# Kernel tuning notes

Measured on AMD Instinct MI355X. Metric: run time of the kernel, lower is better.

Reference implementation:

```python
import jax, jax.numpy as jnp
import numpy as np

W, E, D, NL, NC = 2048, 256, 512, 4, 5
DI, DS, DR, DC = 1024, 64, 32, 4  # d_inner=2*D, d_state, dt_rank=ceil(D/16), d_conv


def setup_inputs() -> dict:
    key = jax.random.key(0)
    ks = jax.random.split(key, 24)
    s = 0.02
    byte_sequence = jax.random.randint(ks[0], (2, W), 0, 256, dtype=jnp.int32)
    p = {
        "byte_sequence": byte_sequence,
        "byte_embed": jax.random.normal(ks[1], (256, E)) * s,
        "pos_embed": jax.random.normal(ks[2], (W, E)) * s,
        "in_w": jax.random.normal(ks[3], (D, E)) * s,
        "in_b": jnp.zeros((D,)),
        "ln_g": jnp.ones((NL, D)),
        "ln_b": jnp.zeros((NL, D)),
        "m_in_w": jax.random.normal(ks[4], (NL, 2 * DI, D)) * s,
        "conv_w": jax.random.normal(ks[5], (NL, DI, DC)) * s,
        "conv_b": jnp.zeros((NL, DI)),
        "xp_w": jax.random.normal(ks[6], (NL, DR + 2 * DS, DI)) * s,
        "dt_w": jax.random.normal(ks[7], (NL, DI, DR)) * s,
        "dt_b": jnp.full((NL, DI), -4.6),  # softplus(-4.6) ~ 0.01, in [dt_min, dt_max]
        "A_log": jnp.broadcast_to(jnp.log(jnp.arange(1.0, DS + 1.0)), (NL, DI, DS)) + 0.0,
        "Dp": jnp.ones((NL, DI)),
        "m_out_w": jax.random.normal(ks[8], (NL, D, DI)) * s,
        "h1_w": jax.random.normal(ks[9], (256, D)) * s,
        "h1_b": jnp.zeros((256,)),
        "h2_w": jax.random.normal(ks[10], (128, 256)) * s,
        "h2_b": jnp.zeros((128,)),
        "h3_w": jax.random.normal(ks[11], (NC, 128)) * s,
        "h3_b": jnp.zeros((NC,)),
    }
    return p


def _layernorm(x, g, b, eps=1e-5):
    mu = jnp.mean(x, axis=-1, keepdims=True)
    var = jnp.mean((x - mu) ** 2, axis=-1, keepdims=True)
    return (x - mu) * jax.lax.rsqrt(var + eps) * g + b


def _mamba(x, in_w, cw, cb, xp_w, dt_w, dt_b, A_log, Dp_, out_w):
    B, L, _ = x.shape
    xr = x @ in_w.T                       # [B,L,2*DI]
    xs, res = xr[..., :DI], xr[..., DI:]
    # causal depthwise conv1d over L
    xc = jnp.transpose(xs, (0, 2, 1))     # [B,DI,L]
    xc = jax.lax.conv_general_dilated(xc, cw[:, None, :], (1,), [(DC - 1, 0)], feature_group_count=DI)
    xs = jax.nn.silu(jnp.transpose(xc + cb[None, :, None], (0, 2, 1)))  # [B,L,DI]
    xdbl = xs @ xp_w.T                    # [B,L,DR+2*DS]
    dt, Bm, Cm = xdbl[..., :DR], xdbl[..., DR:DR + DS], xdbl[..., DR + DS:]
    delta = jax.nn.softplus(dt @ dt_w.T + dt_b)  # [B,L,DI]
    A = -jnp.exp(A_log)                   # [DI,DS]

    def step(h, inp):
        d_t, B_t, C_t, x_t = inp          # [B,DI],[B,DS],[B,DS],[B,DI]
        dA = jnp.exp(d_t[:, :, None] * A)             # [B,DI,DS]
        h = dA * h + (d_t * x_t)[:, :, None] * B_t[:, None, :]
        y = jnp.einsum('bds,bs->bd', h, C_t)
        return h, y

    h0 = jnp.zeros((B, DI, DS), x.dtype)
    seq = (jnp.swapaxes(delta, 0, 1), jnp.swapaxes(Bm, 0, 1), jnp.swapaxes(Cm, 0, 1), jnp.swapaxes(xs, 0, 1))
    _, ys = jax.lax.scan(step, h0, seq)   # ys: [L,B,DI]
    y = jnp.swapaxes(ys, 0, 1) + xs * Dp_
    y = y * jax.nn.silu(res)
    return y @ out_w.T


def reference(byte_sequence, byte_embed, pos_embed, in_w, in_b, ln_g, ln_b, m_in_w, conv_w, conv_b, xp_w, dt_w, dt_b, A_log, Dp, m_out_w, h1_w, h1_b, h2_w, h2_b, h3_w, h3_b):
    B, L = byte_sequence.shape
    x = byte_embed[byte_sequence] + pos_embed[None, :L]  # [B,L,E]
    x = x @ in_w.T + in_b                                # [B,L,D]
    for i in range(NL):
        res = x
        h = _layernorm(x, ln_g[i], ln_b[i])
        h = _mamba(h, m_in_w[i], conv_w[i], conv_b[i], xp_w[i], dt_w[i], dt_b[i], A_log[i], Dp[i], m_out_w[i])
        x = h + res
    h = jax.nn.relu(x @ h1_w.T + h1_b)
    h = jax.nn.relu(h @ h2_w.T + h2_b)
    return h @ h3_w.T + h3_b
```

## Files before the change

### kernel.cpp

```cpp
#include <hip/hip_runtime.h>
#include <hip/hip_bf16.h>

#define WLEN 2048
#define EDIM 256
#define DDIM 512
#define NLAYER 4
#define NCLS 5
#define DI 1024
#define DS 64
#define DR 32
#define DC 4
#define BB 2
#define TOK (BB*WLEN)
#define XD (DR + 2*DS)
#define CL 128
#define NCH (WLEN/CL)
#define LOG2E 1.44269504f

typedef __bf16 bf16x8 __attribute__((ext_vector_type(8)));
typedef float  f32x4  __attribute__((ext_vector_type(4)));

static __device__ __forceinline__ unsigned short f2bf(float f) {
    union { float f; unsigned u; } v; v.f = f;
    unsigned r = v.u + 0x7fffu + ((v.u >> 16) & 1u);
    return (unsigned short)(r >> 16);
}

__global__ __launch_bounds__(256) void embed_k(const int* __restrict__ seq,
    const float* __restrict__ be, const float* __restrict__ pe,
    float* __restrict__ out)
{
    int idx = blockIdx.x * 256 + threadIdx.x;
    int e  = idx & (EDIM - 1);
    int bl = idx >> 8;
    int l  = bl & (WLEN - 1);
    int tok = seq[bl];
    out[idx] = be[tok * EDIM + e] + pe[l * EDIM + e];
}

__global__ __launch_bounds__(256) void ln_k(const float* __restrict__ x,
    const float* __restrict__ g, const float* __restrict__ b,
    unsigned short* __restrict__ out)
{
    int row  = blockIdx.x * 4 + (threadIdx.x >> 6);
    int lane = threadIdx.x & 63;
    const float* xp = x + (size_t)row * DDIM;
    float v[8];
    float s = 0.f;
#pragma unroll
    for (int i = 0; i < 8; i++) { v[i] = xp[lane + 64 * i]; s += v[i]; }
#pragma unroll
    for (int off = 32; off; off >>= 1) s += __shfl_xor(s, off, 64);
    float mu = s * (1.f / 512.f);
    float s2 = 0.f;
#pragma unroll
    for (int i = 0; i < 8; i++) { float d = v[i] - mu; s2 += d * d; }
#pragma unroll
    for (int off = 32; off; off >>= 1) s2 += __shfl_xor(s2, off, 64);
    float rs = rsqrtf(s2 * (1.f / 512.f) + 1e-5f);
#pragma unroll
    for (int i = 0; i < 8; i++) {
        int c = lane + 64 * i;
        out[(size_t)row * DDIM + c] = f2bf((v[i] - mu) * rs * g[c] + b[c]);
    }
}

__global__ __launch_bounds__(256) void conv_silu_k(const float* __restrict__ xr,
    const float* __restrict__ cw, const float* __restrict__ cb,
    float* __restrict__ xs)
{
    int idx = blockIdx.x * 256 + threadIdx.x;
    int d  = idx & (DI - 1);
    int bl = idx >> 10;
    int l  = bl & (WLEN - 1);
    float acc = cb[d];
    const float* wp = cw + d * DC;
#pragma unroll
    for (int k = 0; k < DC; k++) {
        int ls = l - (DC - 1) + k;
        if (ls >= 0)
            acc = fmaf(xr[((size_t)(bl - (DC - 1) + k)) * (2 * DI) + d], wp[k], acc);
    }
    xs[idx] = acc / (1.f + __expf(-acc));
}

__global__ __launch_bounds__(256) void f2bf_k(const float* __restrict__ in,
    unsigned short* __restrict__ out, int n)
{
    int i = blockIdx.x * 256 + threadIdx.x;
    if (i < n) out[i] = f2bf(in[i]);
}

__global__ __launch_bounds__(256) void trans_CT_k(const float* __restrict__ xdbl,
    float* __restrict__ CT)
{
    __shared__ float tile[64][65];
    int bt = blockIdx.x, b = blockIdx.z;
    int col = threadIdx.x & 63, rr = threadIdx.x >> 6;
#pragma unroll
    for (int k = 0; k < 16; k++) {
        int i = k * 4 + rr;
        tile[i][col] = xdbl[((size_t)(b * WLEN + bt * 64 + i)) * XD + DR + DS + col];
    }
    __syncthreads();
#pragma unroll
    for (int k = 0; k < 16; k++) {
        int ss = k * 4 + rr;
        CT[((size_t)(b * DS + ss)) * WLEN + bt * 64 + col] = tile[col][ss];
    }
}

__global__ __launch_bounds__(256) void trans_y_k(const float* __restrict__ yT,
    unsigned short* __restrict__ ybf)
{
    __shared__ float tile[64][65];
    int bt = blockIdx.x, bd = blockIdx.y, b = blockIdx.z;
    int col = threadIdx.x & 63, rr = threadIdx.x >> 6;
#pragma unroll
    for (int k = 0; k < 16; k++) {
        int i = k * 4 + rr;
        tile[i][col] = yT[((size_t)(b * DI + bd * 64 + i)) * WLEN + bt * 64 + col];
    }
    __syncthreads();
#pragma unroll
    for (int k = 0; k < 16; k++) {
        int tt = k * 4 + rr;
        ybf[((size_t)(b * WLEN + bt * 64 + tt)) * DI + bd * 64 + col] = f2bf(tile[col][tt]);
    }
}

#define SU 8

#define LOADG1(T0, dlt, xv, Bt, Ct)                                      \
  _Pragma("unroll")                                                      \
  for (int u = 0; u < SU; u++) {                                         \
    size_t bl = base + (size_t)(T0) + u;                                 \
    dlt[u] = delta[bl * DI + d];                                         \
    xv[u]  = xs[bl * DI + d];                                            \
    Bt[u]  = xdbl[bl * XD + DR + lane];                                  \
    Ct[u]  = xdbl[bl * XD + DR + DS + lane];                             \
  }

#define COMPG1(T0, dlt, xv, Bt, Ct)                                      \
  {                                                                      \
    float dA[SU], p[SU], cds[SU];                                        \
    _Pragma("unroll")                                                    \
    for (int u = 0; u < SU; u++) dA[u] = __expf(dlt[u] * Aa);            \
    _Pragma("unroll")                                                    \
    for (int u = 0; u < SU; u++) {                                       \
      hst = fmaf(dA[u], hst, dlt[u] * xv[u] * Bt[u]);                    \
      p[u] = hst * Ct[u];                                                \
    }                                                                    \
    if (lane == 0) {                                                     \
      _Pragma("unroll")                                                  \
      for (int u = 0; u < SU; u++) p[u] = fmaf(xv[u], Dpd, p[u]);        \
    }                                                                    \
    cds[0] = cd + dlt[0];                                                \
    _Pragma("unroll")                                                    \
    for (int u = 1; u < SU; u++) cds[u] = cds[u - 1] + dlt[u];           \
    cd = cds[SU - 1];                                                    \
    _Pragma("unroll")                                                    \
    for (int u = 0; u < SU; u++)                                         \
      if (lane == u) cdT[tbase + (size_t)(T0) + u] = cds[u];             \
    _Pragma("unroll")                                                    \
    for (int u = 0; u < SU; u++) wred[u * 64 + lane] = p[u];             \
    float4 q0 = *(const float4*)&wred[(lane >> 3) * 64 + (lane & 7) * 8];     \
    float4 q1 = *(const float4*)&wred[(lane >> 3) * 64 + (lane & 7) * 8 + 4]; \
    float sred = ((q0.x + q0.y) + (q0.z + q0.w)) +                       \
                 ((q1.x + q1.y) + (q1.z + q1.w));                        \
    sred += __shfl_xor(sred, 1, 64);                                     \
    sred += __shfl_xor(sred, 2, 64);                                     \
    sred += __shfl_xor(sred, 4, 64);                                     \
    if ((lane & 7) == 0) zT[tbase + (size_t)(T0) + (lane >> 3)] = sred;  \
  }

__global__ __launch_bounds__(256) void scan1_k(
    const float* __restrict__ delta,
    const float* __restrict__ xdbl,
    const float* __restrict__ xs,
    const float* __restrict__ A_log,
    const float* __restrict__ Dp,
    float* __restrict__ zT,
    float* __restrict__ cdT,
    float* __restrict__ Hbuf,
    float* __restrict__ Sbuf)
{
    __shared__ float red[4 * SU * 64];
    int wv   = threadIdx.x >> 6;
    float* wred = red + wv * (SU * 64);
    int wid  = blockIdx.x * 4 + wv;
    int lane = threadIdx.x & 63;
    int c  = wid & (NCH - 1);
    int bd = wid >> 4;
    int d  = bd & (DI - 1);
    float Aa  = -__expf(A_log[d * DS + lane]);
    float Dpd = Dp[d];
    float hst = 0.f, cd = 0.f;
    size_t base  = (size_t)(bd >> 10) * WLEN + (size_t)c * CL;
    size_t tbase = (size_t)bd * WLEN + (size_t)c * CL;

    float da[SU], xa[SU], Ba[SU], Ca[SU];
    float db[SU], xb[SU], Bb[SU], Cb[SU];

    LOADG1(0, da, xa, Ba, Ca)
    for (int t0 = 0; t0 < CL; t0 += 2 * SU) {
        LOADG1(t0 + SU, db, xb, Bb, Cb)
        COMPG1(t0, da, xa, Ba, Ca)
        if (t0 + 2 * SU < CL)
            LOADG1(t0 + 2 * SU, da, xa, Ba, Ca)
        COMPG1(t0 + SU, db, xb, Bb, Cb)
    }
    Hbuf[(size_t)wid * DS + lane] = hst;
    if (lane == 0) Sbuf[wid] = cd;
}

__global__ __launch_bounds__(256) void scan2_k(
    const float* __restrict__ Hbuf, const float* __restrict__ Sbuf,
    const float* __restrict__ A_log, float* __restrict__ h0buf)
{
    int bd   = blockIdx.x * 4 + (threadIdx.x >> 6);
    int lane = threadIdx.x & 63;
    int d = bd & (DI - 1);
    float Aa = -__expf(A_log[d * DS + lane]);
    float h = 0.f;
#pragma unroll
    for (int c = 0; c < NCH; c++) {
        size_t i = (size_t)bd * NCH + c;
        h0buf[i * DS + lane] = h;
        h = __expf(Aa * Sbuf[i]) * h + Hbuf[i * DS + lane];
    }
}

static __device__ __forceinline__ float lanef(float v, int s) {
    return __uint_as_float(__builtin_amdgcn_readlane(__float_as_uint(v), s));
}

__global__ __launch_bounds__(256) void scan3_k(
    const float* __restrict__ zT,
    const float* __restrict__ cdT,
    const float* __restrict__ rT,
    const float* __restrict__ CT,
    const float* __restrict__ A_log,
    const float* __restrict__ h0buf,
    float* __restrict__ yT)
{
    int wid  = blockIdx.x * 4 + (threadIdx.x >> 6);
    int lane = threadIdx.x & 63;
    int c  = wid & (NCH - 1);
    int bd = wid >> 4;
    int d  = bd & (DI - 1);
    int b  = bd >> 10;
    float Kv  = -__expf(A_log[d * DS + lane]) * LOG2E;
    float h0v = h0buf[(size_t)wid * DS + lane];
    size_t rowb = (size_t)bd * WLEN;
    const float* CTb = CT + (size_t)b * DS * WLEN;

#pragma unroll
    for (int pass = 0; pass < CL / 64; pass++) {
        int t = c * CL + pass * 64 + lane;
        float cd = cdT[rowb + t];
        float z  = zT[rowb + t];
        float r  = rT[rowb + t];
        float c0 = 0.f, c1 = 0.f, c2 = 0.f, c3 = 0.f;
#pragma unroll
        for (int s = 0; s < DS; s += 4) {
            float C0 = CTb[(size_t)(s + 0) * WLEN + t];
            float C1 = CTb[(size_t)(s + 1) * WLEN + t];
            float C2 = CTb[(size_t)(s + 2) * WLEN + t];
            float C3 = CTb[(size_t)(s + 3) * WLEN + t];
            c0 = fmaf(C0 * lanef(h0v, s + 0), exp2f(lanef(Kv, s + 0) * cd), c0);
            c1 = fmaf(C1 * lanef(h0v, s + 1), exp2f(lanef(Kv, s + 1) * cd), c1);
            c2 = fmaf(C2 * lanef(h0v, s + 2), exp2f(lanef(Kv, s + 2) * cd), c2);
            c3 = fmaf(C3 * lanef(h0v, s + 3), exp2f(lanef(Kv, s + 3) * cd), c3);
        }
        float corr = (c0 + c1) + (c2 + c3);
        float yv = (z + corr) * (r / (1.f + __expf(-r)));
        yT[rowb + t] = yv;
    }
}

template<int EPI>
__global__ __launch_bounds__(256) void gemm_bf16(
    const unsigned short* __restrict__ A,
    const unsigned short* __restrict__ W,
    const float* __restrict__ resid,
    float* __restrict__ C,
    float* __restrict__ rT,
    int M, int N, int K)
{
    __shared__ unsigned short As[4 * 128 * 8];
    __shared__ unsigned short Bs[4 * 128 * 8];
    const int tid = threadIdx.x;
    const int bm = blockIdx.x * 128, bn = blockIdx.y * 128;
    const int l = tid & 63, w = tid >> 6;
    const int wm = (w >> 1) * 64, wn = (w & 1) * 64;
    const int srow = tid >> 1, shalf = tid & 1;
    const int kq = l >> 4, lr = l & 15;

    f32x4 acc[4][4];
#pragma unroll
    for (int i = 0; i < 4; i++)
#pragma unroll
        for (int j = 0; j < 4; j++)
            acc[i][j] = f32x4{0.f, 0.f, 0.f, 0.f};

    for (int k0 = 0; k0 < K; k0 += 32) {
        const uint4* ga = (const uint4*)(A + (size_t)(bm + srow) * K + k0 + shalf * 16);
        uint4 a0 = ga[0], a1 = ga[1];
        const uint4* gb = (const uint4*)(W + (size_t)(bn + srow) * K + k0 + shalf * 16);
        uint4 b0 = gb[0], b1 = gb[1];
        __syncthreads();
        int kg = shalf * 2;
        *(uint4*)&As[((kg    ) * 128 + srow) * 8] = a0;
        *(uint4*)&As[((kg + 1) * 128 + srow) * 8] = a1;
        *(uint4*)&Bs[((kg    ) * 128 + srow) * 8] = b0;
        *(uint4*)&Bs[((kg + 1) * 128 + srow) * 8] = b1;
        __syncthreads();
        bf16x8 av[4], bv[4];
#pragma unroll
        for (int mf = 0; mf < 4; mf++)
            av[mf] = *(const bf16x8*)&As[(kq * 128 + wm + mf * 16 + lr) * 8];
#pragma unroll
        for (int nf = 0; nf < 4; nf++)
            bv[nf] = *(const bf16x8*)&Bs[(kq * 128 + wn + nf * 16 + lr) * 8];
#pragma unroll
        for (int mf = 0; mf < 4; mf++)
#pragma unroll
            for (int nf = 0; nf < 4; nf++)
                acc[mf][nf] = __builtin_amdgcn_mfma_f32_16x16x32_bf16(
                    av[mf], bv[nf], acc[mf][nf], 0, 0, 0);
    }
#pragma unroll
    for (int mf = 0; mf < 4; mf++) {
#pragma unroll
        for (int nf = 0; nf < 4; nf++) {
            int n  = bn + wn + nf * 16 + lr;
            int m0 = bm + wm + mf * 16 + kq * 4;
            if (EPI == 5 && n >= DI) {
                float4 val = make_float4(acc[mf][nf][0], acc[mf][nf][1],
                                         acc[mf][nf][2], acc[mf][nf][3]);
                int b = m0 >> 11, ll = m0 & (WLEN - 1);
                *(float4*)&rT[((size_t)((b << 10) + (n - DI))) * WLEN + ll] = val;
            } else {
#pragma unroll
                for (int r = 0; r < 4; r++) {
                    int m = m0 + r;
                    float v = acc[mf][nf][r];
                    if (EPI == 4) v += resid[(size_t)m * N + n];
                    C[(size_t)m * N + n] = v;
                }
            }
        }
    }
}

template<int EPI>
__global__ __launch_bounds__(256) void gemm_nt(
    const float* __restrict__ A, int lda,
    const float* __restrict__ W, int ldw,
    const float* __restrict__ bias,
    float* __restrict__ C, int ldc,
    int M, int N, int K)
{
    __shared__ float As[16][64];
    __shared__ float Ws[16][64];
    const int tid = threadIdx.x;
    const int tx = tid & 15;
    const int ty = tid >> 4;
    const int bm = blockIdx.x * 64;
    const int bn = blockIdx.y * 64;
    const int lr = tid >> 2;
    const int lc = (tid & 3) << 2;
    float acc[4][4] = {};
    for (int k0 = 0; k0 < K; k0 += 16) {
        float4 av = *(const float4*)(A + (size_t)(bm + lr) * lda + (k0 + lc));
        float4 wv = make_float4(0.f, 0.f, 0.f, 0.f);
        if (bn + lr < N)
            wv = *(const float4*)(W + (size_t)(bn + lr) * ldw + (k0 + lc));
        As[lc + 0][lr] = av.x; As[lc + 1][lr] = av.y;
        As[lc + 2][lr] = av.z; As[lc + 3][lr] = av.w;
        Ws[lc + 0][lr] = wv.x; Ws[lc + 1][lr] = wv.y;
        Ws[lc + 2][lr] = wv.z; Ws[lc + 3][lr] = wv.w;
        __syncthreads();
#pragma unroll
        for (int k = 0; k < 16; ++k) {
            float4 a = *(const float4*)&As[k][ty * 4];
            float4 w = *(const float4*)&Ws[k][tx * 4];
            float aa[4] = {a.x, a.y, a.z, a.w};
            float ww[4] = {w.x, w.y, w.z, w.w};
#pragma unroll
            for (int i = 0; i < 4; i++)
#pragma unroll
                for (int j = 0; j < 4; j++)
                    acc[i][j] = fmaf(aa[i], ww[j], acc[i][j]);
        }
        __syncthreads();
    }
#pragma unroll
    for (int i = 0; i < 4; i++) {
        int m = bm + ty * 4 + i;
#pragma unroll
        for (int j = 0; j < 4; j++) {
            int n = bn + tx * 4 + j;
            if (n >= N) continue;
            float v = acc[i][j];
            if (EPI == 1 || EPI == 2 || EPI == 3) v += bias[n];
            if (EPI == 2) v = fmaxf(v, 0.f);
            if (EPI == 3) v = fmaxf(v, 0.f) + log1pf(__expf(-fabsf(v)));
            C[(size_t)m * ldc + n] = v;
        }
    }
}

extern "C" void kernel_launch(void* const* d_in, const int* in_sizes, int n_in,
                              void* d_out, int out_size, void* d_ws, size_t ws_size,
                              hipStream_t stream)
{
    const int*   seq        = (const int*)d_in[0];
    const float* byte_embed = (const float*)d_in[1];
    const float* pos_embed  = (const float*)d_in[2];
    const float* in_w       = (const float*)d_in[3];
    const float* in_b       = (const float*)d_in[4];
    const float* ln_g       = (const float*)d_in[5];
    const float* ln_b       = (const float*)d_in[6];
    const float* m_in_w     = (const float*)d_in[7];
    const float* conv_w     = (const float*)d_in[8];
    const float* conv_b     = (const float*)d_in[9];
    const float* xp_w       = (const float*)d_in[10];
    const float* dt_w       = (const float*)d_in[11];
    const float* dt_b       = (const float*)d_in[12];
    const float* A_log      = (const float*)d_in[13];
    const float* Dp         = (const float*)d_in[14];
    const float* m_out_w    = (const float*)d_in[15];
    const float* h1_w       = (const float*)d_in[16];
    const float* h1_b       = (const float*)d_in[17];
    const float* h2_w       = (const float*)d_in[18];
    const float* h2_b       = (const float*)d_in[19];
    const float* h3_w       = (const float*)d_in[20];
    const float* h3_b       = (const float*)d_in[21];
    float* out = (float*)d_out;

    float* ws = (float*)d_ws;
    size_t off = 0;
    float* xe    = ws + off; off += (size_t)TOK * EDIM;
    float* x     = ws + off; off += (size_t)TOK * DDIM;
    float* xr    = ws + off; off += (size_t)TOK * 2 * DI;
    float* xs    = ws + off; off += (size_t)TOK * DI;
    float* xdbl  = ws + off; off += (size_t)TOK * XD;
    float* delta = ws + off; off += (size_t)TOK * DI;
    float* zT    = ws + off; off += (size_t)BB * DI * WLEN;
    float* cdT   = ws + off; off += (size_t)BB * DI * WLEN;
    float* rT    = ws + off; off += (size_t)BB * DI * WLEN;
    float* CT    = ws + off; off += (size_t)BB * DS * WLEN;
    float* Hbuf  = ws + off; off += (size_t)BB * DI * NCH * DS;
    float* h0buf = ws + off; off += (size_t)BB * DI * NCH * DS;
    float* Sbuf  = ws + off; off += (size_t)BB * DI * NCH;
    unsigned short* h_bf  = (unsigned short*)(ws + off); off += (size_t)TOK * DDIM / 2;
    unsigned short* y_bf  = (unsigned short*)(ws + off); off += (size_t)TOK * DI / 2;
    unsigned short* wmi_bf = (unsigned short*)(ws + off); off += (size_t)NLAYER * 2 * DI * DDIM / 2;
    unsigned short* wmo_bf = (unsigned short*)(ws + off); off += (size_t)NLAYER * DDIM * DI / 2;
    float* yT = delta;
    float* t1 = xe;
    float* t2 = (float*)h_bf;

    {
        int n1 = NLAYER * 2 * DI * DDIM;
        f2bf_k<<<(n1 + 255) / 256, 256, 0, stream>>>(m_in_w, wmi_bf, n1);
        int n2 = NLAYER * DDIM * DI;
        f2bf_k<<<(n2 + 255) / 256, 256, 0, stream>>>(m_out_w, wmo_bf, n2);
    }

    embed_k<<<TOK * EDIM / 256, 256, 0, stream>>>(seq, byte_embed, pos_embed, xe);
    gemm_nt<1><<<dim3(TOK/64, DDIM/64), 256, 0, stream>>>(
        xe, EDIM, in_w, EDIM, in_b, x, DDIM, TOK, DDIM, EDIM);

    for (int i = 0; i < NLAYER; i++) {
        const float* lg  = ln_g  + (size_t)i * DDIM;
        const float* lb  = ln_b  + (size_t)i * DDIM;
        const unsigned short* miw = wmi_bf + (size_t)i * 2 * DI * DDIM;
        const float* cw  = conv_w + (size_t)i * DI * DC;
        const float* cb  = conv_b + (size_t)i * DI;
        const float* xpw = xp_w  + (size_t)i * XD * DI;
        const float* dtw = dt_w  + (size_t)i * DI * DR;
        const float* dtb = dt_b  + (size_t)i * DI;
        const float* al  = A_log + (size_t)i * DI * DS;
        const float* dp  = Dp    + (size_t)i * DI;
        const unsigned short* mow = wmo_bf + (size_t)i * DDIM * DI;

        ln_k<<<TOK/4, 256, 0, stream>>>(x, lg, lb, h_bf);
        gemm_bf16<5><<<dim3(TOK/128, 2*DI/128), 256, 0, stream>>>(
            h_bf, miw, nullptr, xr, rT, TOK, 2*DI, DDIM);
        conv_silu_k<<<TOK * DI / 256, 256, 0, stream>>>(xr, cw, cb, xs);
        gemm_nt<0><<<dim3(TOK/64, (XD+63)/64), 256, 0, stream>>>(
            xs, DI, xpw, DI, nullptr, xdbl, XD, TOK, XD, DI);
        trans_CT_k<<<dim3(WLEN/64, 1, BB), 256, 0, stream>>>(xdbl, CT);
        gemm_nt<3><<<dim3(TOK/64, DI/64), 256, 0, stream>>>(
            xdbl, XD, dtw, DR, dtb, delta, DI, TOK, DI, DR);

        scan1_k<<<(BB*DI*NCH)/4, 256, 0, stream>>>(
            delta, xdbl, xs, al, dp, zT, cdT, Hbuf, Sbuf);
        scan2_k<<<(BB*DI)/4, 256, 0, stream>>>(Hbuf, Sbuf, al, h0buf);
        scan3_k<<<(BB*DI*NCH)/4, 256, 0, stream>>>(
            zT, cdT, rT, CT, al, h0buf, yT);
        trans_y_k<<<dim3(WLEN/64, DI/64, BB), 256, 0, stream>>>(yT, y_bf);

        gemm_bf16<4><<<dim3(TOK/128, DDIM/128), 256, 0, stream>>>(
            y_bf, mow, x, x, nullptr, TOK, DDIM, DI);
    }

    gemm_nt<2><<<dim3(TOK/64, 256/64), 256, 0, stream>>>(
        x, DDIM, h1_w, DDIM, h1_b, t1, 256, TOK, 256, DDIM);
    gemm_nt<2><<<dim3(TOK/64, 2), 256, 0, stream>>>(
        t1, 256, h2_w, 256, h2_b, t2, 128, TOK, 128, 256);
    gemm_nt<1><<<dim3(TOK/64, 1), 256, 0, stream>>>(
        t2, 128, h3_w, 128, h3_b, out, NCLS, TOK, NCLS, 128);
}
```

Baseline: 1.934 ms.

## Switch Mamba intermediates to channel-major layout to vectorize scan and conv

```diff
diff --git a/kernel.cpp b/kernel.cpp
--- a/kernel.cpp
+++ b/kernel.cpp
@@ -65,23 +65,42 @@
     }
 }
 
-__global__ __launch_bounds__(256) void conv_silu_k(const float* __restrict__ xr,
+__global__ __launch_bounds__(256) void conv_t_k(const float* __restrict__ xcT,
     const float* __restrict__ cw, const float* __restrict__ cb,
-    float* __restrict__ xs)
-{
-    int idx = blockIdx.x * 256 + threadIdx.x;
-    int d  = idx & (DI - 1);
-    int bl = idx >> 10;
-    int l  = bl & (WLEN - 1);
-    float acc = cb[d];
-    const float* wp = cw + d * DC;
-#pragma unroll
-    for (int k = 0; k < DC; k++) {
-        int ls = l - (DC - 1) + k;
-        if (ls >= 0)
-            acc = fmaf(xr[((size_t)(bl - (DC - 1) + k)) * (2 * DI) + d], wp[k], acc);
-    }
-    xs[idx] = acc / (1.f + __expf(-acc));
+    float* __restrict__ xsT)
+{
+    int gid  = blockIdx.x * 256 + threadIdx.x;
+    int row  = gid >> 9;
+    int col0 = (gid & 511) << 3;
+    int l0   = col0 & (WLEN - 1);
+    const float* src = xcT + (size_t)row * TOK + col0;
+    float xw[12];
+    if (l0 > 0) {
+        float4 a = *(const float4*)(src - 4);
+        xw[0] = a.x; xw[1] = a.y; xw[2] = a.z; xw[3] = a.w;
+    } else {
+        xw[0] = xw[1] = xw[2] = xw[3] = 0.f;
+    }
+    float4 m0 = *(const float4*)src;
+    float4 m1 = *(const float4*)(src + 4);
+    xw[4] = m0.x; xw[5] = m0.y; xw[6] = m0.z; xw[7] = m0.w;
+    xw[8] = m1.x; xw[9] = m1.y; xw[10] = m1.z; xw[11] = m1.w;
+    float w0 = cw[row * DC + 0], w1 = cw[row * DC + 1];
+    float w2 = cw[row * DC + 2], w3 = cw[row * DC + 3];
+    float bias = cb[row];
+    float o[8];
+#pragma unroll
+    for (int u = 0; u < 8; u++) {
+        float a = bias;
+        a = fmaf(w0, xw[u + 1], a);
+        a = fmaf(w1, xw[u + 2], a);
+        a = fmaf(w2, xw[u + 3], a);
+        a = fmaf(w3, xw[u + 4], a);
+        o[u] = a / (1.f + __expf(-a));
+    }
+    float* dst = xsT + (size_t)row * TOK + col0;
+    *(float4*)dst       = make_float4(o[0], o[1], o[2], o[3]);
+    *(float4*)(dst + 4) = make_float4(o[4], o[5], o[6], o[7]);
 }
 
 __global__ __launch_bounds__(256) void f2bf_k(const float* __restrict__ in,
@@ -89,25 +108,6 @@
 {
     int i = blockIdx.x * 256 + threadIdx.x;
     if (i < n) out[i] = f2bf(in[i]);
-}
-
-__global__ __launch_bounds__(256) void trans_CT_k(const float* __restrict__ xdbl,
-    float* __restrict__ CT)
-{
-    __shared__ float tile[64][65];
-    int bt = blockIdx.x, b = blockIdx.z;
-    int col = threadIdx.x & 63, rr = threadIdx.x >> 6;
-#pragma unroll
-    for (int k = 0; k < 16; k++) {
-        int i = k * 4 + rr;
-        tile[i][col] = xdbl[((size_t)(b * WLEN + bt * 64 + i)) * XD + DR + DS + col];
-    }
-    __syncthreads();
-#pragma unroll
-    for (int k = 0; k < 16; k++) {
-        int ss = k * 4 + rr;
-        CT[((size_t)(b * DS + ss)) * WLEN + bt * 64 + col] = tile[col][ss];
-    }
 }
 
 __global__ __launch_bounds__(256) void trans_y_k(const float* __restrict__ yT,
@@ -119,7 +119,7 @@
 #pragma unroll
     for (int k = 0; k < 16; k++) {
         int i = k * 4 + rr;
-        tile[i][col] = yT[((size_t)(b * DI + bd * 64 + i)) * WLEN + bt * 64 + col];
+        tile[i][col] = yT[(size_t)(bd * 64 + i) * TOK + b * WLEN + bt * 64 + col];
     }
     __syncthreads();
 #pragma unroll
@@ -132,13 +132,15 @@
 #define SU 8
 
 #define LOADG1(T0, dlt, xv, Bt, Ct)                                      \
-  _Pragma("unroll")                                                      \
-  for (int u = 0; u < SU; u++) {                                         \
-    size_t bl = base + (size_t)(T0) + u;                                 \
-    dlt[u] = delta[bl * DI + d];                                         \
-    xv[u]  = xs[bl * DI + d];                                            \
-    Bt[u]  = xdbl[bl * XD + DR + lane];                                  \
-    Ct[u]  = xdbl[bl * XD + DR + DS + lane];                             \
+  {                                                                      \
+    *(float4*)&dlt[0] = *(const float4*)&dRow[(T0)];                     \
+    *(float4*)&dlt[4] = *(const float4*)&dRow[(T0) + 4];                 \
+    *(float4*)&xv[0]  = *(const float4*)&xRow[(T0)];                     \
+    *(float4*)&xv[4]  = *(const float4*)&xRow[(T0) + 4];                 \
+    *(float4*)&Bt[0]  = *(const float4*)&BRow[(T0)];                     \
+    *(float4*)&Bt[4]  = *(const float4*)&BRow[(T0) + 4];                 \
+    *(float4*)&Ct[0]  = *(const float4*)&CRow[(T0)];                     \
+    *(float4*)&Ct[4]  = *(const float4*)&CRow[(T0) + 4];                 \
   }
 
 #define COMPG1(T0, dlt, xv, Bt, Ct)                                      \
@@ -149,19 +151,16 @@
     _Pragma("unroll")                                                    \
     for (int u = 0; u < SU; u++) {                                       \
       hst = fmaf(dA[u], hst, dlt[u] * xv[u] * Bt[u]);                    \
-      p[u] = hst * Ct[u];                                                \
-    }                                                                    \
-    if (lane == 0) {                                                     \
-      _Pragma("unroll")                                                  \
-      for (int u = 0; u < SU; u++) p[u] = fmaf(xv[u], Dpd, p[u]);        \
+      p[u] = fmaf(xv[u], Dp0, hst * Ct[u]);                              \
     }                                                                    \
     cds[0] = cd + dlt[0];                                                \
     _Pragma("unroll")                                                    \
     for (int u = 1; u < SU; u++) cds[u] = cds[u - 1] + dlt[u];           \
     cd = cds[SU - 1];                                                    \
-    _Pragma("unroll")                                                    \
-    for (int u = 0; u < SU; u++)                                         \
-      if (lane == u) cdT[tbase + (size_t)(T0) + u] = cds[u];             \
+    if (lane == 0) {                                                     \
+      *(float4*)&cdRow[(T0)]     = make_float4(cds[0], cds[1], cds[2], cds[3]); \
+      *(float4*)&cdRow[(T0) + 4] = make_float4(cds[4], cds[5], cds[6], cds[7]); \
+    }                                                                    \
     _Pragma("unroll")                                                    \
     for (int u = 0; u < SU; u++) wred[u * 64 + lane] = p[u];             \
     float4 q0 = *(const float4*)&wred[(lane >> 3) * 64 + (lane & 7) * 8];     \
@@ -171,13 +170,13 @@
     sred += __shfl_xor(sred, 1, 64);                                     \
     sred += __shfl_xor(sred, 2, 64);                                     \
     sred += __shfl_xor(sred, 4, 64);                                     \
-    if ((lane & 7) == 0) zT[tbase + (size_t)(T0) + (lane >> 3)] = sred;  \
+    if ((lane & 7) == 0) zRow[(T0) + (lane >> 3)] = sred;                \
   }
 
 __global__ __launch_bounds__(256) void scan1_k(
-    const float* __restrict__ delta,
-    const float* __restrict__ xdbl,
-    const float* __restrict__ xs,
+    const float* __restrict__ deltaT,
+    const float* __restrict__ xdblT,
+    const float* __restrict__ xsT,
     const float* __restrict__ A_log,
     const float* __restrict__ Dp,
     float* __restrict__ zT,
@@ -193,11 +192,17 @@
     int c  = wid & (NCH - 1);
     int bd = wid >> 4;
     int d  = bd & (DI - 1);
+    int b  = bd >> 10;
+    size_t col0 = (size_t)b * WLEN + (size_t)c * CL;
+    const float* dRow = deltaT + (size_t)d * TOK + col0;
+    const float* xRow = xsT    + (size_t)d * TOK + col0;
+    const float* BRow = xdblT + (size_t)(DR + lane) * TOK + col0;
+    const float* CRow = xdblT + (size_t)(DR + DS + lane) * TOK + col0;
+    float* zRow  = zT  + (size_t)d * TOK + col0;
+    float* cdRow = cdT + (size_t)d * TOK + col0;
     float Aa  = -__expf(A_log[d * DS + lane]);
-    float Dpd = Dp[d];
+    float Dp0 = (lane == 0) ? Dp[d] : 0.f;
     float hst = 0.f, cd = 0.f;
-    size_t base  = (size_t)(bd >> 10) * WLEN + (size_t)c * CL;
-    size_t tbase = (size_t)bd * WLEN + (size_t)c * CL;
 
     float da[SU], xa[SU], Ba[SU], Ca[SU];
     float db[SU], xb[SU], Bb[SU], Cb[SU];
@@ -239,7 +244,7 @@
     const float* __restrict__ zT,
     const float* __restrict__ cdT,
     const float* __restrict__ rT,
-    const float* __restrict__ CT,
+    const float* __restrict__ xdblT,
     const float* __restrict__ A_log,
     const float* __restrict__ h0buf,
     float* __restrict__ yT)
@@ -252,8 +257,8 @@
     int b  = bd >> 10;
     float Kv  = -__expf(A_log[d * DS + lane]) * LOG2E;
     float h0v = h0buf[(size_t)wid * DS + lane];
-    size_t rowb = (size_t)bd * WLEN;
-    const float* CTb = CT + (size_t)b * DS * WLEN;
+    size_t rowb = (size_t)d * TOK + (size_t)b * WLEN;
+    const float* Cb = xdblT + (size_t)(DR + DS) * TOK + (size_t)b * WLEN;
 
 #pragma unroll
     for (int pass = 0; pass < CL / 64; pass++) {
@@ -264,10 +269,10 @@
         float c0 = 0.f, c1 = 0.f, c2 = 0.f, c3 = 0.f;
 #pragma unroll
         for (int s = 0; s < DS; s += 4) {
-            float C0 = CTb[(size_t)(s + 0) * WLEN + t];
-            float C1 = CTb[(size_t)(s + 1) * WLEN + t];
-            float C2 = CTb[(size_t)(s + 2) * WLEN + t];
-            float C3 = CTb[(size_t)(s + 3) * WLEN + t];
+            float C0 = Cb[(size_t)(s + 0) * TOK + t];
+            float C1 = Cb[(size_t)(s + 1) * TOK + t];
+            float C2 = Cb[(size_t)(s + 2) * TOK + t];
+            float C3 = Cb[(size_t)(s + 3) * TOK + t];
             c0 = fmaf(C0 * lanef(h0v, s + 0), exp2f(lanef(Kv, s + 0) * cd), c0);
             c1 = fmaf(C1 * lanef(h0v, s + 1), exp2f(lanef(Kv, s + 1) * cd), c1);
             c2 = fmaf(C2 * lanef(h0v, s + 2), exp2f(lanef(Kv, s + 2) * cd), c2);
@@ -285,7 +290,8 @@
     const unsigned short* __restrict__ W,
     const float* __restrict__ resid,
     float* __restrict__ C,
-    float* __restrict__ rT,
+    float* __restrict__ T0buf,
+    float* __restrict__ T1buf,
     int M, int N, int K)
 {
     __shared__ unsigned short As[4 * 128 * 8];
@@ -336,11 +342,12 @@
         for (int nf = 0; nf < 4; nf++) {
             int n  = bn + wn + nf * 16 + lr;
             int m0 = bm + wm + mf * 16 + kq * 4;
-            if (EPI == 5 && n >= DI) {
+            if (EPI == 5) {
                 float4 val = make_float4(acc[mf][nf][0], acc[mf][nf][1],
                                          acc[mf][nf][2], acc[mf][nf][3]);
-                int b = m0 >> 11, ll = m0 & (WLEN - 1);
-                *(float4*)&rT[((size_t)((b << 10) + (n - DI))) * WLEN + ll] = val;
+                float* dst = (n < DI) ? &T0buf[(size_t)n * TOK + m0]
+                                      : &T1buf[(size_t)(n - DI) * TOK + m0];
+                *(float4*)dst = val;
             } else {
 #pragma unroll
                 for (int r = 0; r < 4; r++) {
@@ -351,6 +358,64 @@
                 }
             }
         }
+    }
+}
+
+template<int EPI>
+__global__ __launch_bounds__(256) void gemm_nn(
+    const float* __restrict__ A,
+    const float* __restrict__ B,
+    const float* __restrict__ bias,
+    float* __restrict__ C,
+    int M, int N, int K)
+{
+    __shared__ float As[16][64];
+    __shared__ float Bs[16][64];
+    const int tid = threadIdx.x;
+    const int tx = tid & 15, ty = tid >> 4;
+    const int bm = blockIdx.x * 64, bn = blockIdx.y * 64;
+    const int arow = tid >> 2, ak = (tid & 3) << 2;
+    const int brow = tid & 15, bn4 = (tid >> 4) << 2;
+    float acc[4][4] = {};
+    for (int k0 = 0; k0 < K; k0 += 16) {
+        float4 av = make_float4(0.f, 0.f, 0.f, 0.f);
+        if (bm + arow < M)
+            av = *(const float4*)&A[(size_t)(bm + arow) * K + k0 + ak];
+        float4 bv = *(const float4*)&B[(size_t)(k0 + brow) * N + bn + bn4];
+        __syncthreads();
+        As[ak + 0][arow] = av.x; As[ak + 1][arow] = av.y;
+        As[ak + 2][arow] = av.z; As[ak + 3][arow] = av.w;
+        *(float4*)&Bs[brow][bn4] = bv;
+        __syncthreads();
+#pragma unroll
+        for (int k = 0; k < 16; ++k) {
+            float4 a = *(const float4*)&As[k][ty * 4];
+            float4 w = *(const float4*)&Bs[k][tx * 4];
+            float aa[4] = {a.x, a.y, a.z, a.w};
+            float ww[4] = {w.x, w.y, w.z, w.w};
+#pragma unroll
+            for (int i = 0; i < 4; i++)
+#pragma unroll
+                for (int j = 0; j < 4; j++)
+                    acc[i][j] = fmaf(aa[i], ww[j], acc[i][j]);
+        }
+        __syncthreads();
+    }
+#pragma unroll
+    for (int i = 0; i < 4; i++) {
+        int m = bm + ty * 4 + i;
+        if (m >= M) continue;
+        float vv[4];
+#pragma unroll
+        for (int j = 0; j < 4; j++) {
+            float v = acc[i][j];
+            if (EPI == 3) {
+                v += bias[m];
+                v = fmaxf(v, 0.f) + log1pf(__expf(-fabsf(v)));
+            }
+            vv[j] = v;
+        }
+        *(float4*)&C[(size_t)m * N + bn + tx * 4] = make_float4(vv[0], vv[1], vv[2], vv[3]);
     }
 }
 
@@ -404,9 +469,8 @@
             int n = bn + tx * 4 + j;
             if (n >= N) continue;
             float v = acc[i][j];
-            if (EPI == 1 || EPI == 2 || EPI == 3) v += bias[n];
+            v += bias[n];
             if (EPI == 2) v = fmaxf(v, 0.f);
-            if (EPI == 3) v = fmaxf(v, 0.f) + log1pf(__expf(-fabsf(v)));
             C[(size_t)m * ldc + n] = v;
         }
     }
@@ -442,24 +506,23 @@
 
     float* ws = (float*)d_ws;
     size_t off = 0;
-    float* xe    = ws + off; off += (size_t)TOK * EDIM;
-    float* x     = ws + off; off += (size_t)TOK * DDIM;
-    float* xr    = ws + off; off += (size_t)TOK * 2 * DI;
-    float* xs    = ws + off; off += (size_t)TOK * DI;
-    float* xdbl  = ws + off; off += (size_t)TOK * XD;
-    float* delta = ws + off; off += (size_t)TOK * DI;
-    float* zT    = ws + off; off += (size_t)BB * DI * WLEN;
-    float* cdT   = ws + off; off += (size_t)BB * DI * WLEN;
-    float* rT    = ws + off; off += (size_t)BB * DI * WLEN;
-    float* CT    = ws + off; off += (size_t)BB * DS * WLEN;
-    float* Hbuf  = ws + off; off += (size_t)BB * DI * NCH * DS;
-    float* h0buf = ws + off; off += (size_t)BB * DI * NCH * DS;
-    float* Sbuf  = ws + off; off += (size_t)BB * DI * NCH;
-    unsigned short* h_bf  = (unsigned short*)(ws + off); off += (size_t)TOK * DDIM / 2;
-    unsigned short* y_bf  = (unsigned short*)(ws + off); off += (size_t)TOK * DI / 2;
+    float* xe     = ws + off; off += (size_t)TOK * EDIM;
+    float* x      = ws + off; off += (size_t)TOK * DDIM;
+    float* xcT    = ws + off; off += (size_t)DI * TOK;
+    float* xsT    = ws + off; off += (size_t)DI * TOK;
+    float* xdblT  = ws + off; off += (size_t)XD * TOK;
+    float* deltaT = ws + off; off += (size_t)DI * TOK;
+    float* zT     = ws + off; off += (size_t)DI * TOK;
+    float* cdT    = ws + off; off += (size_t)DI * TOK;
+    float* rT     = ws + off; off += (size_t)DI * TOK;
+    float* Hbuf   = ws + off; off += (size_t)BB * DI * NCH * DS;
+    float* h0buf  = ws + off; off += (size_t)BB * DI * NCH * DS;
+    float* Sbuf   = ws + off; off += (size_t)BB * DI * NCH;
+    unsigned short* h_bf   = (unsigned short*)(ws + off); off += (size_t)TOK * DDIM / 2;
+    unsigned short* y_bf   = (unsigned short*)(ws + off); off += (size_t)TOK * DI / 2;
     unsigned short* wmi_bf = (unsigned short*)(ws + off); off += (size_t)NLAYER * 2 * DI * DDIM / 2;
     unsigned short* wmo_bf = (unsigned short*)(ws + off); off += (size_t)NLAYER * DDIM * DI / 2;
-    float* yT = delta;
+    float* yT = deltaT;
     float* t1 = xe;
     float* t2 = (float*)h_bf;
 
@@ -489,23 +552,22 @@
 
         ln_k<<<TOK/4, 256, 0, stream>>>(x, lg, lb, h_bf);
         gemm_bf16<5><<<dim3(TOK/128, 2*DI/128), 256, 0, stream>>>(
-            h_bf, miw, nullptr, xr, rT, TOK, 2*DI, DDIM);
-        conv_silu_k<<<TOK * DI / 256, 256, 0, stream>>>(xr, cw, cb, xs);
-        gemm_nt<0><<<dim3(TOK/64, (XD+63)/64), 256, 0, stream>>>(
-            xs, DI, xpw, DI, nullptr, xdbl, XD, TOK, XD, DI);
-        trans_CT_k<<<dim3(WLEN/64, 1, BB), 256, 0, stream>>>(xdbl, CT);
-        gemm_nt<3><<<dim3(TOK/64, DI/64), 256, 0, stream>>>(
-            xdbl, XD, dtw, DR, dtb, delta, DI, TOK, DI, DR);
+            h_bf, miw, nullptr, nullptr, xcT, rT, TOK, 2*DI, DDIM);
+        conv_t_k<<<(DI * TOK / 8) / 256, 256, 0, stream>>>(xcT, cw, cb, xsT);
+        gemm_nn<0><<<dim3((XD + 63) / 64, TOK / 64), 256, 0, stream>>>(
+            xpw, xsT, nullptr, xdblT, XD, TOK, DI);
+        gemm_nn<3><<<dim3(DI / 64, TOK / 64), 256, 0, stream>>>(
+            dtw, xdblT, dtb, deltaT, DI, TOK, DR);
 
         scan1_k<<<(BB*DI*NCH)/4, 256, 0, stream>>>(
-            delta, xdbl, xs, al, dp, zT, cdT, Hbuf, Sbuf);
+            deltaT, xdblT, xsT, al, dp, zT, cdT, Hbuf, Sbuf);
         scan2_k<<<(BB*DI)/4, 256, 0, stream>>>(Hbuf, Sbuf, al, h0buf);
         scan3_k<<<(BB*DI*NCH)/4, 256, 0, stream>>>(
-            zT, cdT, rT, CT, al, h0buf, yT);
+            zT, cdT, rT, xdblT, al, h0buf, yT);
         trans_y_k<<<dim3(WLEN/64, DI/64, BB), 256, 0, stream>>>(yT, y_bf);
 
         gemm_bf16<4><<<dim3(TOK/128, DDIM/128), 256, 0, stream>>>(
-            y_bf, mow, x, x, nullptr, TOK, DDIM, DI);
+            y_bf, mow, x, x, nullptr, nullptr, TOK, DDIM, DI);
     }
 
     gemm_nt<2><<<dim3(TOK/64, 256/64), 256, 0, stream>>>(
```

Measured after the change: 2.589 ms. +33.9%, slower.
